# Optimization experiments

Measured on AMD Instinct MI355X. Metric: run time of the kernel, lower is better.

## Reference

```python
import jax, jax.numpy as jnp
import numpy as np

BZ, C, H, W = 4, 512, 64, 64

def setup_inputs() -> dict:
    key = jax.random.key(0)
    k1, k2 = jax.random.split(key)
    inp = jax.random.normal(k1, (BZ, C, H, W), dtype=jnp.float32)
    mask = jax.random.randint(k2, (BZ, 1, H, W), 0, 2, dtype=jnp.int32)  # 1 = hole
    return {"input": inp, "mask": mask}

def reference(input, mask):
    bz, c, h, w = input.shape
    c2 = c // 2
    hw = h * w
    former = input[:, :c2].reshape(bz, c2, hw)   # decoder features
    latter = input[:, c2:].reshape(bz, c2, hw)   # encoder skip features
    # flag: 1 where masked (hole). shift_sz=1, stride=1, mask_thred=1 => flag == mask
    flag = (mask.reshape(bz, hw) >= 1)
    # cosine similarity between all per-pixel latter features (normalize once)
    norm = jnp.sqrt(jnp.sum(latter * latter, axis=1, keepdims=True))
    lat_n = latter / (norm + 1e-8)
    sim = jnp.einsum('bci,bcj->bij', lat_n, lat_n)  # [bz, hw(query), hw(key)]
    # only known (non-masked) pixels are valid shift sources (keys)
    NEG = jnp.float32(-1e9)
    sim = jnp.where(flag[:, None, :], NEG, sim)
    src_idx = jnp.argmax(sim, axis=2)  # [bz, hw] best known source per pixel
    # shift: copy former feature from matched known pixel into masked positions
    shifted = jnp.take_along_axis(former, src_idx[:, None, :], axis=2)  # [bz, c2, hw]
    shifted = jnp.where(flag[:, None, :], shifted, jnp.float32(0.0))
    out = jnp.concatenate([former, latter, shifted], axis=1)  # [bz, 3*c2, hw]
    return out.reshape(bz, 3 * c2, h, w)
```

## Files before the change

kernel.cpp:

```cpp
#include <hip/hip_runtime.h>


#define HW 4096
#define C2 256
#define BZd 4
#define TQ 32
#define NK 2
#define BT 256
#define SLK 512
#define NSL_MAX 8
#define QT_MAX 128
#define P1_GRID 1024

__device__ __forceinline__ unsigned ordf(float f) {
  unsigned u = __float_as_uint(f);
  return (u & 0x80000000u) ? ~u : (u | 0x80000000u);
}

__device__ __forceinline__ unsigned long long shfl_down_u64(unsigned long long v, int off) {
  unsigned lo = (unsigned)v, hi = (unsigned)(v >> 32);
  lo = __shfl_down(lo, off, 64);
  hi = __shfl_down(hi, off, 64);
  return ((unsigned long long)hi << 32) | lo;
}

__global__ void prep_kernel(const float* __restrict__ in, const int* __restrict__ mask,
                            float* __restrict__ inv, int* __restrict__ qcnt,
                            int* __restrict__ kcnt, int* __restrict__ qlist,
                            int* __restrict__ klist, int* __restrict__ srcmap) {
  int bid = blockIdx.x, t = threadIdx.x;
  if (bid < 256) {
    __shared__ float sred[4][64];
    int p = t & 63, g = t >> 6;
    int idx = bid * 64 + p;
    int b = idx >> 12, j = idx & (HW - 1);
    const float* base = in + ((size_t)b * 512 + C2 + g * 64) * HW + j;
    float ss = 0.f;
#pragma unroll 8
    for (int c = 0; c < 64; ++c) { float v = base[(size_t)c * HW]; ss = fmaf(v, v, ss); }
    sred[g][p] = ss;
    __syncthreads();
    if (g == 0) {
      float s0 = ((sred[0][p] + sred[1][p]) + sred[2][p]) + sred[3][p];
      inv[idx] = 1.0f / (sqrtf(s0) + 1e-8f);
    }
  } else {
    int b = bid - 256;
    __shared__ int s[256];
    const int* m = mask + b * HW;
    int base = t * 16;
    int fl = 0, cq = 0;
#pragma unroll
    for (int i = 0; i < 16; ++i) { int f = (m[base + i] >= 1); fl |= f << i; cq += f; }
    s[t] = cq; __syncthreads();
    for (int off = 1; off < 256; off <<= 1) {
      int v = (t >= off) ? s[t - off] : 0;
      __syncthreads(); s[t] += v; __syncthreads();
    }
    int total = s[255];
    int qp = s[t] - cq;
    int kp = base - qp;
    for (int i = 0; i < 16; ++i) {
      int j = base + i;
      if ((fl >> i) & 1) qlist[b * HW + qp++] = j;
      else               klist[b * HW + kp++] = j;
      srcmap[b * HW + j] = -1;
    }
    if (t == 0) { qcnt[b] = total; kcnt[b] = HW - total; }
  }
}

__global__ void pack_kernel(const float* __restrict__ in, const float* __restrict__ inv,
                            const int* __restrict__ qcnt, const int* __restrict__ kcnt,
                            const int* __restrict__ qlist, const int* __restrict__ klist,
                            float* __restrict__ kpack, float* __restrict__ qpack) {
  __shared__ float slat[HW];
  __shared__ float sinv[HW];
  int t = threadIdx.x;
  int c = blockIdx.x, b = blockIdx.y;
  const float4* lat4 = (const float4*)(in + ((size_t)b * 512 + C2 + c) * HW);
  const float4* inv4 = (const float4*)(inv + (size_t)b * HW);
#pragma unroll
  for (int i = 0; i < 4; ++i) {
    int p = i * 256 + t;
    ((float4*)slat)[p] = lat4[p];
    ((float4*)sinv)[p] = inv4[p];
  }
  int kc = kcnt[b], nq = qcnt[b];
  const int* kl = klist + b * HW;
  const int* ql = qlist + b * HW;
  float* kdst = kpack + (size_t)(b * C2 + c) * HW;
  float* qdst = qpack + (size_t)(b * C2 + c) * HW;
  __syncthreads();
#pragma unroll
  for (int i = 0; i < 4; ++i) {
    int jj = (i * 256 + t) * 4;
    int4 k4 = *(const int4*)(kl + jj);
    int4 q4 = *(const int4*)(ql + jj);
    float4 kv, qv;
    kv.x = (jj + 0 < kc) ? slat[k4.x] * sinv[k4.x] : 0.f;
    kv.y = (jj + 1 < kc) ? slat[k4.y] * sinv[k4.y] : 0.f;
    kv.z = (jj + 2 < kc) ? slat[k4.z] * sinv[k4.z] : 0.f;
    kv.w = (jj + 3 < kc) ? slat[k4.w] * sinv[k4.w] : 0.f;
    qv.x = (jj + 0 < nq) ? slat[q4.x] : 0.f;
    qv.y = (jj + 1 < nq) ? slat[q4.y] : 0.f;
    qv.z = (jj + 2 < nq) ? slat[q4.z] : 0.f;
    qv.w = (jj + 3 < nq) ? slat[q4.w] : 0.f;
    *(float4*)(kdst + jj) = kv;
    *(float4*)(qdst + jj) = qv;
  }
}

__device__ __forceinline__ void decode_id(unsigned idx,
    int nt0, int nt1, int nt2,
    int q0, int q1, int q2, int q3,
    int k0c, int k1c, int k2c, int k3c,
    int& b, int& sl, int& qtile, int& kc) {
  int qtn;
  b = 0; qtn = q0; kc = k0c;
  if (idx >= (unsigned)nt0) {
    idx -= nt0; b = 1; qtn = q1; kc = k1c;
    if (idx >= (unsigned)nt1) {
      idx -= nt1; b = 2; qtn = q2; kc = k2c;
      if (idx >= (unsigned)nt2) { idx -= nt2; b = 3; qtn = q3; kc = k3c; }
    }
  }
  sl = (int)(idx / (unsigned)qtn);
  qtile = (int)(idx - (unsigned)sl * (unsigned)qtn);
}

template <int TQL>
__device__ __forceinline__ void run_item(
    const float* __restrict__ qpack, const float* __restrict__ kpack,
    unsigned long long* __restrict__ partials,
    unsigned long long (*red)[TQ],
    int b, int sl, int qtile, int qoff, int kc,
    int t, int lane, int wid) {
  int qstart = (qtile << 5) + qoff;
  int kbase = (sl << 9) + (t << 1);

  const float* qb = qpack + ((size_t)b * C2) * HW + qstart;
  const float* kcol = kpack + ((size_t)b * C2) * HW + kbase;

  float acc[NK][TQL];
#pragma unroll
  for (int r = 0; r < NK; ++r)
#pragma unroll
    for (int q = 0; q < TQL; ++q) acc[r][q] = 0.f;

  float2 k0 = *(const float2*)(kcol);
  float2 k1 = *(const float2*)(kcol + HW);
#pragma unroll 2
  for (int c = 0; c < C2; ++c) {
    float2 kq = k0;
    k0 = k1;
    int cp = c + 2; if (cp > C2 - 1) cp = C2 - 1;
    k1 = *(const float2*)(kcol + (size_t)cp * HW);
    float kv[NK] = {kq.x, kq.y};
    const float* qc_ = qb + (size_t)c * HW;
#pragma unroll
    for (int i = 0; i < TQL; ++i) {
      float qv = qc_[i];
#pragma unroll
      for (int r = 0; r < NK; ++r)
        acc[r][i] = fmaf(kv[r], qv, acc[r][i]);
    }
  }

#pragma unroll
  for (int q = 0; q < TQL; ++q) {
    unsigned long long v = 0ull;
#pragma unroll
    for (int r = 0; r < NK; ++r) {
      int kk = kbase + r;
      if (kk < kc) {
        unsigned long long pk =
            ((unsigned long long)ordf(acc[r][q]) << 32) | (unsigned)(0xFFFFFFFFu - (unsigned)kk);
        if (pk > v) v = pk;
      }
    }
#pragma unroll
    for (int off = 32; off >= 1; off >>= 1) {
      unsigned long long o = shfl_down_u64(v, off);
      if (o > v) v = o;
    }
    if (lane == 0) red[wid][q] = v;
  }
  __syncthreads();
  if (t < TQL) {
    unsigned long long v = red[0][t];
#pragma unroll
    for (int ww = 1; ww < 4; ++ww) if (red[ww][t] > v) v = red[ww][t];
    partials[(((size_t)b * NSL_MAX + sl) * QT_MAX + qtile) * TQ + qoff + t] = v;
  }
  __syncthreads();
}

__global__ __launch_bounds__(BT, 4) void argmax_pass1(
    const float* __restrict__ qpack, const float* __restrict__ kpack,
    const int* __restrict__ qcnt, const int* __restrict__ kcnt,
    unsigned long long* __restrict__ partials) {
  int k0c = kcnt[0], k1c = kcnt[1], k2c = kcnt[2], k3c = kcnt[3];
  int s0 = (k0c + SLK - 1) >> 9, s1 = (k1c + SLK - 1) >> 9;
  int s2 = (k2c + SLK - 1) >> 9, s3 = (k3c + SLK - 1) >> 9;
  int q0 = (qcnt[0] + TQ - 1) >> 5, q1 = (qcnt[1] + TQ - 1) >> 5;
  int q2 = (qcnt[2] + TQ - 1) >> 5, q3 = (qcnt[3] + TQ - 1) >> 5;
  int nt0 = q0 * s0, nt1 = q1 * s1, nt2 = q2 * s2, nt3 = q3 * s3;
  unsigned total = (unsigned)(nt0 + nt1 + nt2 + nt3);
  unsigned S = gridDim.x;
  unsigned F = total / S;
  unsigned fullN = F * S;
  unsigned R = total - fullN;

  int t = threadIdx.x;
  int lane = t & 63, wid = t >> 6;
  __shared__ unsigned long long red[4][TQ];

  for (unsigned w = blockIdx.x; w < fullN; w += S) {
    int b, sl, qtile, kc;
    decode_id(w, nt0, nt1, nt2, q0, q1, q2, q3, k0c, k1c, k2c, k3c, b, sl, qtile, kc);
    run_item<TQ>(qpack, kpack, partials, red, b, sl, qtile, 0, kc, t, lane, wid);
  }
  for (unsigned qi = blockIdx.x; qi < 4u * R; qi += S) {
    unsigned id = fullN + (qi >> 2);
    int sub = (int)(qi & 3u);
    int b, sl, qtile, kc;
    decode_id(id, nt0, nt1, nt2, q0, q1, q2, q3, k0c, k1c, k2c, k3c, b, sl, qtile, kc);
    run_item<8>(qpack, kpack, partials, red, b, sl, qtile, sub * 8, kc, t, lane, wid);
  }
}

__global__ void argmax_pass2(const unsigned long long* __restrict__ partials,
                             const int* __restrict__ qcnt, const int* __restrict__ kcnt,
                             const int* __restrict__ qlist, const int* __restrict__ klist,
                             int* __restrict__ srcmap) {
  int idx = blockIdx.x * 256 + threadIdx.x;
  int b = idx >> 12, qpos = idx & (HW - 1);
  if (qpos >= qcnt[b]) return;
  int kc = kcnt[b];
  int ns = (kc + SLK - 1) >> 9;
  int qtile = qpos >> 5, q = qpos & (TQ - 1);
  unsigned long long v = 0ull;
  for (int s = 0; s < ns; ++s) {
    unsigned long long p = partials[(((size_t)b * NSL_MAX + s) * QT_MAX + qtile) * TQ + q];
    if (p > v) v = p;
  }
  if (!v) return;
  int kk = (int)(0xFFFFFFFFu - (unsigned)(v & 0xFFFFFFFFull));
  srcmap[b * HW + qlist[b * HW + qpos]] = klist[b * HW + kk];
}

__global__ void out_kernel(const float* __restrict__ in, const int* __restrict__ srcmap,
                           float* __restrict__ out) {
  __shared__ float srow[HW];
  int bid = blockIdx.x;
  int b = bid >> 9, c = bid & 511;
  int t = threadIdx.x;
  const float4* src = (const float4*)(in + ((size_t)b * 512 + c) * HW);
  float4* dst = (float4*)(out + ((size_t)b * 768 + c) * HW);
#pragma unroll
  for (int i = 0; i < 4; ++i) {
    int p = i * 256 + t;
    float4 v = src[p];
    ((float4*)srow)[p] = v;
    dst[p] = v;
  }
  if (c < 256) {
    __syncthreads();
    const int* sm = srcmap + b * HW;
    float4* dst2 = (float4*)(out + ((size_t)b * 768 + 512 + c) * HW);
#pragma unroll
    for (int i = 0; i < 4; ++i) {
      int p = i * 256 + t;
      int j0 = p * 4;
      int4 s4 = *(const int4*)(sm + j0);
      float4 o;
      o.x = (s4.x >= 0) ? srow[s4.x] : 0.f;
      o.y = (s4.y >= 0) ? srow[s4.y] : 0.f;
      o.z = (s4.z >= 0) ? srow[s4.z] : 0.f;
      o.w = (s4.w >= 0) ? srow[s4.w] : 0.f;
      dst2[p] = o;
    }
  }
}

extern "C" void kernel_launch(void* const* d_in, const int* in_sizes, int n_in,
                              void* d_out, int out_size, void* d_ws, size_t ws_size,
                              hipStream_t stream) {
  const float* in = (const float*)d_in[0];
  const int* mask = (const int*)d_in[1];
  float* out = (float*)d_out;

  unsigned long long* partials = (unsigned long long*)d_ws;
  float* kpack = (float*)(partials + (size_t)BZd * NSL_MAX * QT_MAX * TQ);
  float* qpack = kpack + (size_t)BZd * C2 * HW;
  float* inv = qpack + (size_t)BZd * C2 * HW;
  int* qlist = (int*)(inv + BZd * HW);
  int* klist = qlist + BZd * HW;
  int* srcmap = klist + BZd * HW;
  int* qcnt = srcmap + BZd * HW;
  int* kcnt = qcnt + BZd;

  hipLaunchKernelGGL(prep_kernel, dim3(256 + BZd), dim3(256), 0, stream,
                     in, mask, inv, qcnt, kcnt, qlist, klist, srcmap);
  hipLaunchKernelGGL(pack_kernel, dim3(C2, BZd), dim3(256), 0, stream,
                     in, inv, qcnt, kcnt, qlist, klist, kpack, qpack);
  hipLaunchKernelGGL(argmax_pass1, dim3(P1_GRID), dim3(BT), 0, stream,
                     qpack, kpack, qcnt, kcnt, partials);
  hipLaunchKernelGGL(argmax_pass2, dim3(BZd * HW / 256), dim3(256), 0, stream,
                     partials, qcnt, kcnt, qlist, klist, srcmap);
  hipLaunchKernelGGL(out_kernel, dim3(BZd * 512), dim3(256), 0, stream,
                     in, srcmap, out);
}
```

Before: 228.1 us.

## Split tail work items across waves by key quarter instead of query sub-tiles

The leftover work items that do not fill a full grid round are now split so that each wave independently handles a quarter of the key slice across all 32 queries. Previously the whole block processed 8-query sub-tiles, which re-read the full key slice four times. Each wave writes its own partial result, which removes the block-level barrier in the tail. The partials buffer grows by a factor of four, and the second pass recomputes the work-item mapping to decide whether it needs to merge one partial or four.

After: 291.7 us. 1.28x slower.

```diff
diff --git a/kernel.cpp b/kernel.cpp
--- a/kernel.cpp
+++ b/kernel.cpp
@@ -129,24 +129,23 @@
   qtile = (int)(idx - (unsigned)sl * (unsigned)qtn);
 }
 
-template <int TQL>
 __device__ __forceinline__ void run_item(
     const float* __restrict__ qpack, const float* __restrict__ kpack,
     unsigned long long* __restrict__ partials,
     unsigned long long (*red)[TQ],
-    int b, int sl, int qtile, int qoff, int kc,
+    int b, int sl, int qtile, int kc,
     int t, int lane, int wid) {
-  int qstart = (qtile << 5) + qoff;
+  int qstart = qtile << 5;
   int kbase = (sl << 9) + (t << 1);
 
   const float* qb = qpack + ((size_t)b * C2) * HW + qstart;
   const float* kcol = kpack + ((size_t)b * C2) * HW + kbase;
 
-  float acc[NK][TQL];
+  float acc[NK][TQ];
 #pragma unroll
   for (int r = 0; r < NK; ++r)
 #pragma unroll
-    for (int q = 0; q < TQL; ++q) acc[r][q] = 0.f;
+    for (int q = 0; q < TQ; ++q) acc[r][q] = 0.f;
 
   float2 k0 = *(const float2*)(kcol);
   float2 k1 = *(const float2*)(kcol + HW);
@@ -159,7 +158,7 @@
     float kv[NK] = {kq.x, kq.y};
     const float* qc_ = qb + (size_t)c * HW;
 #pragma unroll
-    for (int i = 0; i < TQL; ++i) {
+    for (int i = 0; i < TQ; ++i) {
       float qv = qc_[i];
 #pragma unroll
       for (int r = 0; r < NK; ++r)
@@ -168,7 +167,7 @@
   }
 
 #pragma unroll
-  for (int q = 0; q < TQL; ++q) {
+  for (int q = 0; q < TQ; ++q) {
     unsigned long long v = 0ull;
 #pragma unroll
     for (int r = 0; r < NK; ++r) {
@@ -187,13 +186,70 @@
     if (lane == 0) red[wid][q] = v;
   }
   __syncthreads();
-  if (t < TQL) {
+  if (t < TQ) {
     unsigned long long v = red[0][t];
 #pragma unroll
     for (int ww = 1; ww < 4; ++ww) if (red[ww][t] > v) v = red[ww][t];
-    partials[(((size_t)b * NSL_MAX + sl) * QT_MAX + qtile) * TQ + qoff + t] = v;
+    partials[((((size_t)b * NSL_MAX + sl) * 4 + 0) * QT_MAX + qtile) * TQ + t] = v;
   }
   __syncthreads();
+}
+
+__device__ __forceinline__ void run_subitem(
+    const float* __restrict__ qpack, const float* __restrict__ kpack,
+    unsigned long long* __restrict__ partials,
+    int b, int sl, int qtile, int kq, int kc, int lane) {
+  int qstart = qtile << 5;
+  int kbase = (sl << 9) + (kq << 7) + (lane << 1);
+
+  const float* qb = qpack + ((size_t)b * C2) * HW + qstart;
+  const float* kcol = kpack + ((size_t)b * C2) * HW + kbase;
+
+  float acc[NK][TQ];
+#pragma unroll
+  for (int r = 0; r < NK; ++r)
+#pragma unroll
+    for (int q = 0; q < TQ; ++q) acc[r][q] = 0.f;
+
+  float2 k0 = *(const float2*)(kcol);
+  float2 k1 = *(const float2*)(kcol + HW);
+#pragma unroll 2
+  for (int c = 0; c < C2; ++c) {
+    float2 kqv = k0;
+    k0 = k1;
+    int cp = c + 2; if (cp > C2 - 1) cp = C2 - 1;
+    k1 = *(const float2*)(kcol + (size_t)cp * HW);
+    float kv[NK] = {kqv.x, kqv.y};
+    const float* qc_ = qb + (size_t)c * HW;
+#pragma unroll
+    for (int i = 0; i < TQ; ++i) {
+      float qv = qc_[i];
+#pragma unroll
+      for (int r = 0; r < NK; ++r)
+        acc[r][i] = fmaf(kv[r], qv, acc[r][i]);
+    }
+  }
+
+#pragma unroll
+  for (int q = 0; q < TQ; ++q) {
+    unsigned long long v = 0ull;
+#pragma unroll
+    for (int r = 0; r < NK; ++r) {
+      int kk = kbase + r;
+      if (kk < kc) {
+        unsigned long long pk =
+            ((unsigned long long)ordf(acc[r][q]) << 32) | (unsigned)(0xFFFFFFFFu - (unsigned)kk);
+        if (pk > v) v = pk;
+      }
+    }
+#pragma unroll
+    for (int off = 32; off >= 1; off >>= 1) {
+      unsigned long long o = shfl_down_u64(v, off);
+      if (o > v) v = o;
+    }
+    if (lane == 0)
+      partials[((((size_t)b * NSL_MAX + sl) * 4 + kq) * QT_MAX + qtile) * TQ + q] = v;
+  }
 }
 
 __global__ __launch_bounds__(BT, 4) void argmax_pass1(
@@ -219,14 +275,14 @@
   for (unsigned w = blockIdx.x; w < fullN; w += S) {
     int b, sl, qtile, kc;
     decode_id(w, nt0, nt1, nt2, q0, q1, q2, q3, k0c, k1c, k2c, k3c, b, sl, qtile, kc);
-    run_item<TQ>(qpack, kpack, partials, red, b, sl, qtile, 0, kc, t, lane, wid);
-  }
-  for (unsigned qi = blockIdx.x; qi < 4u * R; qi += S) {
-    unsigned id = fullN + (qi >> 2);
-    int sub = (int)(qi & 3u);
+    run_item(qpack, kpack, partials, red, b, sl, qtile, kc, t, lane, wid);
+  }
+  for (unsigned gw = blockIdx.x * 4u + (unsigned)wid; gw < 4u * R; gw += 4u * S) {
+    unsigned id = fullN + (gw >> 2);
+    int kq = (int)(gw & 3u);
     int b, sl, qtile, kc;
     decode_id(id, nt0, nt1, nt2, q0, q1, q2, q3, k0c, k1c, k2c, k3c, b, sl, qtile, kc);
-    run_item<8>(qpack, kpack, partials, red, b, sl, qtile, sub * 8, kc, t, lane, wid);
+    run_subitem(qpack, kpack, partials, b, sl, qtile, kq, kc, lane);
   }
 }
 
@@ -237,13 +293,37 @@
   int idx = blockIdx.x * 256 + threadIdx.x;
   int b = idx >> 12, qpos = idx & (HW - 1);
   if (qpos >= qcnt[b]) return;
+
+  int k0c = kcnt[0], k1c = kcnt[1], k2c = kcnt[2], k3c = kcnt[3];
+  int s0 = (k0c + SLK - 1) >> 9, s1 = (k1c + SLK - 1) >> 9;
+  int s2 = (k2c + SLK - 1) >> 9, s3 = (k3c + SLK - 1) >> 9;
+  int q0 = (qcnt[0] + TQ - 1) >> 5, q1 = (qcnt[1] + TQ - 1) >> 5;
+  int q2 = (qcnt[2] + TQ - 1) >> 5, q3 = (qcnt[3] + TQ - 1) >> 5;
+  int nt0 = q0 * s0, nt1 = q1 * s1, nt2 = q2 * s2, nt3 = q3 * s3;
+  unsigned total = (unsigned)(nt0 + nt1 + nt2 + nt3);
+  unsigned F = total / P1_GRID;
+  unsigned fullN = F * P1_GRID;
+
   int kc = kcnt[b];
   int ns = (kc + SLK - 1) >> 9;
+  int qtn = (b == 0) ? q0 : (b == 1) ? q1 : (b == 2) ? q2 : q3;
+  int base = (b == 0) ? 0 : (b == 1) ? nt0 : (b == 2) ? (nt0 + nt1) : (nt0 + nt1 + nt2);
   int qtile = qpos >> 5, q = qpos & (TQ - 1);
+
   unsigned long long v = 0ull;
   for (int s = 0; s < ns; ++s) {
-    unsigned long long p = partials[(((size_t)b * NSL_MAX + s) * QT_MAX + qtile) * TQ + q];
-    if (p > v) v = p;
+    unsigned w = (unsigned)(base + s * qtn + qtile);
+    size_t pb = (((size_t)b * NSL_MAX + s) * 4) * QT_MAX;
+    if (w < fullN) {
+      unsigned long long p = partials[(pb + qtile) * TQ + q];
+      if (p > v) v = p;
+    } else {
+#pragma unroll
+      for (int kq = 0; kq < 4; ++kq) {
+        unsigned long long p = partials[(pb + (size_t)kq * QT_MAX + qtile) * TQ + q];
+        if (p > v) v = p;
+      }
+    }
   }
   if (!v) return;
   int kk = (int)(0xFFFFFFFFu - (unsigned)(v & 0xFFFFFFFFull));
@@ -292,7 +372,7 @@
   float* out = (float*)d_out;
 
   unsigned long long* partials = (unsigned long long*)d_ws;
-  float* kpack = (float*)(partials + (size_t)BZd * NSL_MAX * QT_MAX * TQ);
+  float* kpack = (float*)(partials + (size_t)BZd * NSL_MAX * 4 * QT_MAX * TQ);
   float* qpack = kpack + (size_t)BZd * C2 * HW;
   float* inv = qpack + (size_t)BZd * C2 * HW;
   int* qlist = (int*)(inv + BZd * HW);
```

## Use packed float2 FMA in argmax GEMM and overlap passthrough copy with pass1

Applied to the files above, without the earlier changes.

The inner similarity loop now accumulates into two-wide float vectors with elementwise FMA, so the compiler can emit packed FP32 FMA instructions (v_pk_fma_f32) and double arithmetic throughput per instruction. Separately, the former/latter passthrough copy moves out of out_kernel into extra blocks appended to the argmax_pass1 grid. That copy then runs alongside the compute-bound pass and out_kernel only handles the shifted half. The packed accumulators may raise register pressure, and the extra copy blocks compete with the argmax blocks for CUs.

Result: no change. 223.7 us (-1.9%).

```diff
diff --git a/kernel.cpp b/kernel.cpp
--- a/kernel.cpp
+++ b/kernel.cpp
@@ -11,6 +11,9 @@
 #define NSL_MAX 8
 #define QT_MAX 128
 #define P1_GRID 1024
+#define CP_GRID 2048
+
+typedef float v2f __attribute__((ext_vector_type(2)));
 
 __device__ __forceinline__ unsigned ordf(float f) {
   unsigned u = __float_as_uint(f);
@@ -142,11 +145,11 @@
   const float* qb = qpack + ((size_t)b * C2) * HW + qstart;
   const float* kcol = kpack + ((size_t)b * C2) * HW + kbase;
 
-  float acc[NK][TQL];
+  v2f acc[NK][TQL / 2];
 #pragma unroll
   for (int r = 0; r < NK; ++r)
 #pragma unroll
-    for (int q = 0; q < TQL; ++q) acc[r][q] = 0.f;
+    for (int q = 0; q < TQL / 2; ++q) acc[r][q] = (v2f){0.f, 0.f};
 
   float2 k0 = *(const float2*)(kcol);
   float2 k1 = *(const float2*)(kcol + HW);
@@ -156,14 +159,16 @@
     k0 = k1;
     int cp = c + 2; if (cp > C2 - 1) cp = C2 - 1;
     k1 = *(const float2*)(kcol + (size_t)cp * HW);
-    float kv[NK] = {kq.x, kq.y};
-    const float* qc_ = qb + (size_t)c * HW;
-#pragma unroll
-    for (int i = 0; i < TQL; ++i) {
-      float qv = qc_[i];
+    v2f kv2[NK];
+    kv2[0] = (v2f){kq.x, kq.x};
+    kv2[1] = (v2f){kq.y, kq.y};
+    const v2f* qc2 = (const v2f*)(qb + (size_t)c * HW);
+#pragma unroll
+    for (int i = 0; i < TQL / 2; ++i) {
+      v2f qv = qc2[i];
 #pragma unroll
       for (int r = 0; r < NK; ++r)
-        acc[r][i] = fmaf(kv[r], qv, acc[r][i]);
+        acc[r][i] = __builtin_elementwise_fma(kv2[r], qv, acc[r][i]);
     }
   }
 
@@ -174,8 +179,9 @@
     for (int r = 0; r < NK; ++r) {
       int kk = kbase + r;
       if (kk < kc) {
+        float a = (q & 1) ? acc[r][q >> 1].y : acc[r][q >> 1].x;
         unsigned long long pk =
-            ((unsigned long long)ordf(acc[r][q]) << 32) | (unsigned)(0xFFFFFFFFu - (unsigned)kk);
+            ((unsigned long long)ordf(a) << 32) | (unsigned)(0xFFFFFFFFu - (unsigned)kk);
         if (pk > v) v = pk;
       }
     }
@@ -199,7 +205,19 @@
 __global__ __launch_bounds__(BT, 4) void argmax_pass1(
     const float* __restrict__ qpack, const float* __restrict__ kpack,
     const int* __restrict__ qcnt, const int* __restrict__ kcnt,
-    unsigned long long* __restrict__ partials) {
+    unsigned long long* __restrict__ partials,
+    const float* __restrict__ in, float* __restrict__ out) {
+  int t = threadIdx.x;
+  if (blockIdx.x >= P1_GRID) {
+    int bid2 = blockIdx.x - P1_GRID;
+    int b = bid2 >> 9, c = bid2 & 511;
+    const float4* src = (const float4*)(in + ((size_t)b * 512 + c) * HW);
+    float4* dst = (float4*)(out + ((size_t)b * 768 + c) * HW);
+#pragma unroll
+    for (int i = 0; i < 4; ++i) dst[i * 256 + t] = src[i * 256 + t];
+    return;
+  }
+
   int k0c = kcnt[0], k1c = kcnt[1], k2c = kcnt[2], k3c = kcnt[3];
   int s0 = (k0c + SLK - 1) >> 9, s1 = (k1c + SLK - 1) >> 9;
   int s2 = (k2c + SLK - 1) >> 9, s3 = (k3c + SLK - 1) >> 9;
@@ -207,12 +225,11 @@
   int q2 = (qcnt[2] + TQ - 1) >> 5, q3 = (qcnt[3] + TQ - 1) >> 5;
   int nt0 = q0 * s0, nt1 = q1 * s1, nt2 = q2 * s2, nt3 = q3 * s3;
   unsigned total = (unsigned)(nt0 + nt1 + nt2 + nt3);
-  unsigned S = gridDim.x;
+  unsigned S = P1_GRID;
   unsigned F = total / S;
   unsigned fullN = F * S;
   unsigned R = total - fullN;
 
-  int t = threadIdx.x;
   int lane = t & 63, wid = t >> 6;
   __shared__ unsigned long long red[4][TQ];
 
@@ -254,33 +271,25 @@
                            float* __restrict__ out) {
   __shared__ float srow[HW];
   int bid = blockIdx.x;
-  int b = bid >> 9, c = bid & 511;
+  int b = bid >> 8, c = bid & 255;
   int t = threadIdx.x;
   const float4* src = (const float4*)(in + ((size_t)b * 512 + c) * HW);
-  float4* dst = (float4*)(out + ((size_t)b * 768 + c) * HW);
+#pragma unroll
+  for (int i = 0; i < 4; ++i) ((float4*)srow)[i * 256 + t] = src[i * 256 + t];
+  __syncthreads();
+  const int* sm = srcmap + b * HW;
+  float4* dst2 = (float4*)(out + ((size_t)b * 768 + 512 + c) * HW);
 #pragma unroll
   for (int i = 0; i < 4; ++i) {
     int p = i * 256 + t;
-    float4 v = src[p];
-    ((float4*)srow)[p] = v;
-    dst[p] = v;
-  }
-  if (c < 256) {
-    __syncthreads();
-    const int* sm = srcmap + b * HW;
-    float4* dst2 = (float4*)(out + ((size_t)b * 768 + 512 + c) * HW);
-#pragma unroll
-    for (int i = 0; i < 4; ++i) {
-      int p = i * 256 + t;
-      int j0 = p * 4;
-      int4 s4 = *(const int4*)(sm + j0);
-      float4 o;
-      o.x = (s4.x >= 0) ? srow[s4.x] : 0.f;
-      o.y = (s4.y >= 0) ? srow[s4.y] : 0.f;
-      o.z = (s4.z >= 0) ? srow[s4.z] : 0.f;
-      o.w = (s4.w >= 0) ? srow[s4.w] : 0.f;
-      dst2[p] = o;
-    }
+    int j0 = p * 4;
+    int4 s4 = *(const int4*)(sm + j0);
+    float4 o;
+    o.x = (s4.x >= 0) ? srow[s4.x] : 0.f;
+    o.y = (s4.y >= 0) ? srow[s4.y] : 0.f;
+    o.z = (s4.z >= 0) ? srow[s4.z] : 0.f;
+    o.w = (s4.w >= 0) ? srow[s4.w] : 0.f;
+    dst2[p] = o;
   }
 }
 
@@ -305,10 +314,10 @@
                      in, mask, inv, qcnt, kcnt, qlist, klist, srcmap);
   hipLaunchKernelGGL(pack_kernel, dim3(C2, BZd), dim3(256), 0, stream,
                      in, inv, qcnt, kcnt, qlist, klist, kpack, qpack);
-  hipLaunchKernelGGL(argmax_pass1, dim3(P1_GRID), dim3(BT), 0, stream,
-                     qpack, kpack, qcnt, kcnt, partials);
+  hipLaunchKernelGGL(argmax_pass1, dim3(P1_GRID + CP_GRID), dim3(BT), 0, stream,
+                     qpack, kpack, qcnt, kcnt, partials, in, out);
   hipLaunchKernelGGL(argmax_pass2, dim3(BZd * HW / 256), dim3(256), 0, stream,
                      partials, qcnt, kcnt, qlist, klist, srcmap);
-  hipLaunchKernelGGL(out_kernel, dim3(BZd * 512), dim3(256), 0, stream,
+  hipLaunchKernelGGL(out_kernel, dim3(BZd * 256), dim3(256), 0, stream,
                      in, srcmap, out);
 }
```
